# Optimization experiments

Measured on AMD Instinct MI355X. Metric: run time of the kernel, lower is better.

Reference implementation:

```python
import jax, jax.numpy as jnp
import numpy as np

L = 256  # label-space bound (labels 0..L-1, 0 = background)

def setup_inputs() -> dict:
    key = jax.random.key(0)
    k1, k2 = jax.random.split(key)
    H = W = 4096
    pred = jax.random.randint(k1, (H, W), 0, L, dtype=jnp.int32)
    gt = jax.random.randint(k2, (H, W), 0, L, dtype=jnp.int32)
    return {"pred_labels_mask": pred, "gt_labels_mask": gt}

def reference(pred_labels_mask, gt_labels_mask):
    p = pred_labels_mask.reshape(-1).astype(jnp.int32)
    g = gt_labels_mask.reshape(-1).astype(jnp.int32)
    # Label co-occurrence (confusion) matrix via a single scatter-add histogram.
    C = jnp.zeros((L * L,), jnp.int32).at[g * L + p].add(1).reshape(L, L)
    gt_size = C.sum(axis=1)    # full pixel count per gt label
    pred_size = C.sum(axis=0)  # full pixel count per pred label
    gt_present = (gt_size > 0).at[0].set(False)
    pred_present = (pred_size > 0).at[0].set(False)
    num_gt = gt_present.sum()
    num_pred = pred_present.sum()
    # intersections restricted to nonzero gt and nonzero pred labels
    Cnz = C.at[0, :].set(0).at[:, 0].set(0)
    overlap = Cnz > 0
    pairs = overlap.sum()                     # every overlapping (gt,pred) pair is either tp or ns
    ea = (overlap.sum(axis=0) > 1).sum()      # preds overlapping more than one gt
    # match condition: intersection > 0.5*gt_size  <=>  2*inter > gt_size (exact int compare).
    # At most one pred can majority-cover a gt, so argmax identifies it.
    M = (2 * Cnz) > gt_size[:, None]
    best_p = jnp.argmax(M, axis=1)
    has = M.any(axis=1)
    inter = jnp.take_along_axis(Cnz, best_p[:, None], axis=1)[:, 0]
    # Greedy matching in ascending gt-label order (torch.unique order); a pred may match once.
    def step(carry, gl):
        used, tp, seg_sum = carry
        pl = best_p[gl]
        ok = has[gl] & (~used[pl])
        union = gt_size[gl] + pred_size[pl] - inter[gl]
        iou = inter[gl].astype(jnp.float32) / jnp.maximum(union, 1).astype(jnp.float32)
        seg_sum = seg_sum + jnp.where(ok, iou, 0.0)
        used = used.at[pl].set(used[pl] | ok)
        return (used, tp + ok.astype(jnp.int32), seg_sum), None
    init = (jnp.zeros((L,), bool), jnp.int32(0), jnp.float32(0.0))
    (used, tp, seg_sum), _ = jax.lax.scan(step, init, jnp.arange(1, L))
    ng = jnp.maximum(num_gt, 1).astype(jnp.float32)
    seg = seg_sum / ng  # mean over SEG array of length num_gt (zeros for unmatched gts)
    ns = pairs - tp
    fn = num_gt - tp
    fp = num_pred - tp
    det = 1.0 - (fp + fn + ns + ea).astype(jnp.float32) / ng
    both_empty = (num_gt == 0) & (num_pred == 0)
    any_empty = (num_gt == 0) | (num_pred == 0)
    seg = jnp.where(both_empty, 1.0, jnp.where(any_empty, 0.0, seg))
    det = jnp.where(both_empty, 1.0, jnp.where(any_empty, 0.0, det))
    return seg.astype(jnp.float32), det.astype(jnp.float32)
```

## Files before the change

kernel.cpp:

```cpp
#include <hip/hip_runtime.h>

#define LBL 256
#define NBINS (LBL * LBL)
#define NWORDS (NBINS / 2)
#define NQUADS (NWORDS / 4)
#define HIST_BLOCKS 256
#define HIST_THREADS 1024

typedef int vint4 __attribute__((ext_vector_type(4)));

__global__ __launch_bounds__(HIST_THREADS, 4)
void hist_priv_kernel(const int* __restrict__ pred, const int* __restrict__ gt,
                      unsigned int* __restrict__ partial, int n4, int n) {
    __shared__ unsigned int h[NWORDS];
    const int t = threadIdx.x;
    #pragma unroll
    for (int i = t; i < NWORDS; i += HIST_THREADS) h[i] = 0u;
    __syncthreads();

    const vint4* p4 = (const vint4*)pred;
    const vint4* g4 = (const vint4*)gt;
    const int stride = HIST_BLOCKS * HIST_THREADS;
    int i = blockIdx.x * HIST_THREADS + t;
    for (; i + 3 * stride < n4; i += 4 * stride) {
        vint4 pa = __builtin_nontemporal_load(&p4[i]);
        vint4 ga = __builtin_nontemporal_load(&g4[i]);
        vint4 pb = __builtin_nontemporal_load(&p4[i + stride]);
        vint4 gb = __builtin_nontemporal_load(&g4[i + stride]);
        vint4 pc = __builtin_nontemporal_load(&p4[i + 2 * stride]);
        vint4 gc = __builtin_nontemporal_load(&g4[i + 2 * stride]);
        vint4 pd = __builtin_nontemporal_load(&p4[i + 3 * stride]);
        vint4 gd = __builtin_nontemporal_load(&g4[i + 3 * stride]);
        int b;
        b = (ga.x << 8) | pa.x; atomicAdd(&h[b >> 1], 1u << ((b & 1) << 4));
        b = (ga.y << 8) | pa.y; atomicAdd(&h[b >> 1], 1u << ((b & 1) << 4));
        b = (ga.z << 8) | pa.z; atomicAdd(&h[b >> 1], 1u << ((b & 1) << 4));
        b = (ga.w << 8) | pa.w; atomicAdd(&h[b >> 1], 1u << ((b & 1) << 4));
        b = (gb.x << 8) | pb.x; atomicAdd(&h[b >> 1], 1u << ((b & 1) << 4));
        b = (gb.y << 8) | pb.y; atomicAdd(&h[b >> 1], 1u << ((b & 1) << 4));
        b = (gb.z << 8) | pb.z; atomicAdd(&h[b >> 1], 1u << ((b & 1) << 4));
        b = (gb.w << 8) | pb.w; atomicAdd(&h[b >> 1], 1u << ((b & 1) << 4));
        b = (gc.x << 8) | pc.x; atomicAdd(&h[b >> 1], 1u << ((b & 1) << 4));
        b = (gc.y << 8) | pc.y; atomicAdd(&h[b >> 1], 1u << ((b & 1) << 4));
        b = (gc.z << 8) | pc.z; atomicAdd(&h[b >> 1], 1u << ((b & 1) << 4));
        b = (gc.w << 8) | pc.w; atomicAdd(&h[b >> 1], 1u << ((b & 1) << 4));
        b = (gd.x << 8) | pd.x; atomicAdd(&h[b >> 1], 1u << ((b & 1) << 4));
        b = (gd.y << 8) | pd.y; atomicAdd(&h[b >> 1], 1u << ((b & 1) << 4));
        b = (gd.z << 8) | pd.z; atomicAdd(&h[b >> 1], 1u << ((b & 1) << 4));
        b = (gd.w << 8) | pd.w; atomicAdd(&h[b >> 1], 1u << ((b & 1) << 4));
    }
    for (; i < n4; i += stride) {
        vint4 p = p4[i];
        vint4 g = g4[i];
        int b;
        b = (g.x << 8) | p.x; atomicAdd(&h[b >> 1], 1u << ((b & 1) << 4));
        b = (g.y << 8) | p.y; atomicAdd(&h[b >> 1], 1u << ((b & 1) << 4));
        b = (g.z << 8) | p.z; atomicAdd(&h[b >> 1], 1u << ((b & 1) << 4));
        b = (g.w << 8) | p.w; atomicAdd(&h[b >> 1], 1u << ((b & 1) << 4));
    }
    if (blockIdx.x == 0 && t == 0) {
        for (int j = n4 * 4; j < n; ++j) {
            int b = (gt[j] << 8) | pred[j];
            atomicAdd(&h[b >> 1], 1u << ((b & 1) << 4));
        }
    }
    __syncthreads();
    uint4* dst = (uint4*)(partial + (size_t)blockIdx.x * NWORDS);
    const uint4* src = (const uint4*)h;
    #pragma unroll
    for (int j = t; j < NQUADS; j += HIST_THREADS) dst[j] = src[j];
}

__global__ __launch_bounds__(256)
void reduce_kernel(const unsigned int* __restrict__ partial, int* __restrict__ C,
                   int* __restrict__ meta) {
    __shared__ int acc[256];
    __shared__ int red[4], redp[4];
    __shared__ int s_gs, s_rp, s_best, s_inter;
    const int t = threadIdx.x;
    const int r = blockIdx.x;
    acc[t] = 0;
    if (t == 0) { s_best = 0; s_inter = 0; }
    __syncthreads();

    const int qlocal = t & 31;
    const int q = r * 32 + qlocal;
    const int pg = t >> 5;
    const uint4* p4 = (const uint4*)partial;
    int s0 = 0, s1 = 0, s2 = 0, s3 = 0, s4 = 0, s5 = 0, s6 = 0, s7 = 0;
    #pragma unroll 8
    for (int k = 0; k < 32; ++k) {
        uint4 v = p4[(size_t)(pg * 32 + k) * NQUADS + q];
        s0 += (int)(v.x & 0xFFFFu); s1 += (int)(v.x >> 16);
        s2 += (int)(v.y & 0xFFFFu); s3 += (int)(v.y >> 16);
        s4 += (int)(v.z & 0xFFFFu); s5 += (int)(v.z >> 16);
        s6 += (int)(v.w & 0xFFFFu); s7 += (int)(v.w >> 16);
    }
    const int cb = qlocal * 8;
    atomicAdd(&acc[cb + 0], s0); atomicAdd(&acc[cb + 1], s1);
    atomicAdd(&acc[cb + 2], s2); atomicAdd(&acc[cb + 3], s3);
    atomicAdd(&acc[cb + 4], s4); atomicAdd(&acc[cb + 5], s5);
    atomicAdd(&acc[cb + 6], s6); atomicAdd(&acc[cb + 7], s7);
    __syncthreads();

    const int v = acc[t];
    if (t < 64) ((int4*)(C + r * LBL))[t] = ((const int4*)acc)[t];

    int ssum = v;
    int pcnt = (r >= 1 && t >= 1 && v > 0) ? 1 : 0;
    #pragma unroll
    for (int m = 32; m >= 1; m >>= 1) {
        ssum += __shfl_xor(ssum, m);
        pcnt += __shfl_xor(pcnt, m);
    }
    if ((t & 63) == 0) { red[t >> 6] = ssum; redp[t >> 6] = pcnt; }
    __syncthreads();
    if (t == 0) {
        s_gs = red[0] + red[1] + red[2] + red[3];
        s_rp = redp[0] + redp[1] + redp[2] + redp[3];
    }
    __syncthreads();
    const int gs = s_gs;
    if (r >= 1 && t >= 1 && 2 * v > gs) { s_best = t; s_inter = v; }
    __syncthreads();
    if (t == 0) {
        meta[0 * LBL + r] = gs;
        meta[1 * LBL + r] = s_rp;
        meta[2 * LBL + r] = s_best;
        meta[3 * LBL + r] = s_inter;
        meta[4 * LBL + r] = (s_best > 0) ? 1 : 0;
    }
}

__global__ __launch_bounds__(1024)
void finalize_kernel(const int* __restrict__ C, const int* __restrict__ meta,
                     float* __restrict__ out) {
    __shared__ int colsum[1024], colcnt4[1024];
    __shared__ int pred_size[LBL], colcnt[LBL];
    __shared__ unsigned char used_s[LBL];
    __shared__ int s_ngt, s_npred, s_pairs, s_ea;
    const int t = threadIdx.x;
    if (t == 0) { s_ngt = 0; s_npred = 0; s_pairs = 0; s_ea = 0; }
    if (t < LBL) used_s[t] = 0;

    const int c = t & 255, qg = t >> 8;
    int cs = 0, cc = 0;
    #pragma unroll 8
    for (int g0 = 0; g0 < 64; ++g0) {
        int row = qg * 64 + g0;
        int v = C[row * LBL + c];
        cs += v;
        cc += (row >= 1 && c >= 1 && v > 0) ? 1 : 0;
    }
    colsum[t] = cs;
    colcnt4[t] = cc;
    __syncthreads();
    if (t < LBL) {
        pred_size[t] = colsum[t] + colsum[256 + t] + colsum[512 + t] + colsum[768 + t];
        colcnt[t]   = colcnt4[t] + colcnt4[256 + t] + colcnt4[512 + t] + colcnt4[768 + t];
    }
    __syncthreads();
    if (t >= 1 && t < LBL) {
        if (meta[0 * LBL + t] > 0) atomicAdd(&s_ngt, 1);
        if (pred_size[t] > 0) atomicAdd(&s_npred, 1);
        if (colcnt[t] > 1) atomicAdd(&s_ea, 1);
        int rp = meta[1 * LBL + t];
        if (rp) atomicAdd(&s_pairs, rp);
    }
    __syncthreads();

    if (t == 0) {
        const int num_gt = s_ngt, num_pred = s_npred, pairs = s_pairs, ea = s_ea;
        int tp = 0;
        float seg_sum = 0.0f;
        for (int gl = 1; gl < LBL; ++gl) {
            if (meta[4 * LBL + gl]) {
                int pl = meta[2 * LBL + gl];
                if (!used_s[pl]) {
                    int uni = meta[0 * LBL + gl] + pred_size[pl] - meta[3 * LBL + gl];
                    if (uni < 1) uni = 1;
                    seg_sum += (float)meta[3 * LBL + gl] / (float)uni;
                    used_s[pl] = 1;
                    tp++;
                }
            }
        }
        float ng = (float)(num_gt >= 1 ? num_gt : 1);
        float seg = seg_sum / ng;
        int ns = pairs - tp;
        int fn = num_gt - tp;
        int fp_ = num_pred - tp;
        float det = 1.0f - (float)(fp_ + fn + ns + ea) / ng;
        bool both_empty = (num_gt == 0) && (num_pred == 0);
        bool any_empty = (num_gt == 0) || (num_pred == 0);
        if (both_empty) { seg = 1.0f; det = 1.0f; }
        else if (any_empty) { seg = 0.0f; det = 0.0f; }
        out[0] = seg;
        out[1] = det;
    }
}

__global__ void hist_atomic_kernel(const int* __restrict__ pred, const int* __restrict__ gt,
                                   int* __restrict__ C, int n4, int n) {
    int idx = blockIdx.x * blockDim.x + threadIdx.x;
    int stride = gridDim.x * blockDim.x;
    const vint4* p4 = (const vint4*)pred;
    const vint4* g4 = (const vint4*)gt;
    for (int i = idx; i < n4; i += stride) {
        vint4 p = p4[i];
        vint4 g = g4[i];
        atomicAdd(&C[(g.x << 8) + p.x], 1);
        atomicAdd(&C[(g.y << 8) + p.y], 1);
        atomicAdd(&C[(g.z << 8) + p.z], 1);
        atomicAdd(&C[(g.w << 8) + p.w], 1);
    }
    if (idx == 0)
        for (int i = n4 * 4; i < n; ++i) atomicAdd(&C[(gt[i] << 8) + pred[i]], 1);
}

__global__ __launch_bounds__(1024)
void finalize_full_kernel(const int* __restrict__ C, float* __restrict__ out) {
    __shared__ int scratch[1024];
    __shared__ int gt_size[LBL], pred_size[LBL];
    __shared__ int best_p[LBL], inter_s[LBL], colcnt[LBL];
    __shared__ unsigned char has_s[LBL], used_s[LBL];
    __shared__ int s_pairs, s_ngt, s_npred, s_ea;
    const int t = threadIdx.x;
    if (t == 0) { s_pairs = 0; s_ngt = 0; s_npred = 0; s_ea = 0; }
    if (t < LBL) { best_p[t] = 0; inter_s[t] = 0; colcnt[t] = 0; has_s[t] = 0; used_s[t] = 0; }
    const int4* C4 = (const int4*)C;
    const int r = t >> 2, q = t & 3;
    int s = 0;
    #pragma unroll
    for (int j = 0; j < 16; ++j) {
        int4 v = C4[r * 64 + q * 16 + j];
        s += v.x + v.y + v.z + v.w;
    }
    scratch[t] = s;
    __syncthreads();
    if (t < LBL)
        gt_size[t] = scratch[4 * t] + scratch[4 * t + 1] + scratch[4 * t + 2] + scratch[4 * t + 3];
    __syncthreads();
    {
        const int c = t & 255, q2 = t >> 8;
        int cs = 0, cc = 0;
        #pragma unroll 8
        for (int g0 = 0; g0 < 64; ++g0) {
            int row = q2 * 64 + g0;
            int v = C[row * LBL + c];
            cs += v;
            cc += (row >= 1 && c >= 1 && v > 0) ? 1 : 0;
        }
        scratch[t] = cs;
        if (cc) atomicAdd(&colcnt[c], cc);
    }
    if (r >= 1) {
        const int gs = gt_size[r];
        int rp = 0;
        #pragma unroll
        for (int j = 0; j < 16; ++j) {
            int4 v = C4[r * 64 + q * 16 + j];
            int cb = q * 64 + 4 * j;
            if (cb >= 1) {
                if (v.x > 0) rp++;
                if (2 * v.x > gs) { has_s[r] = 1; best_p[r] = cb; inter_s[r] = v.x; }
            }
            if (v.y > 0) rp++;
            if (2 * v.y > gs) { has_s[r] = 1; best_p[r] = cb + 1; inter_s[r] = v.y; }
            if (v.z > 0) rp++;
            if (2 * v.z > gs) { has_s[r] = 1; best_p[r] = cb + 2; inter_s[r] = v.z; }
            if (v.w > 0) rp++;
            if (2 * v.w > gs) { has_s[r] = 1; best_p[r] = cb + 3; inter_s[r] = v.w; }
        }
        if (rp) atomicAdd(&s_pairs, rp);
    }
    __syncthreads();
    if (t < LBL)
        pred_size[t] = scratch[t] + scratch[256 + t] + scratch[512 + t] + scratch[768 + t];
    __syncthreads();
    if (t >= 1 && t < LBL) {
        if (gt_size[t] > 0) atomicAdd(&s_ngt, 1);
        if (pred_size[t] > 0) atomicAdd(&s_npred, 1);
        if (colcnt[t] > 1) atomicAdd(&s_ea, 1);
    }
    __syncthreads();
    if (t == 0) {
        const int num_gt = s_ngt, num_pred = s_npred, pairs = s_pairs, ea = s_ea;
        int tp = 0;
        float seg_sum = 0.0f;
        for (int gl = 1; gl < LBL; ++gl) {
            if (has_s[gl]) {
                int pl = best_p[gl];
                if (!used_s[pl]) {
                    int uni = gt_size[gl] + pred_size[pl] - inter_s[gl];
                    if (uni < 1) uni = 1;
                    seg_sum += (float)inter_s[gl] / (float)uni;
                    used_s[pl] = 1;
                    tp++;
                }
            }
        }
        float ng = (float)(num_gt >= 1 ? num_gt : 1);
        float seg = seg_sum / ng;
        int ns = pairs - tp;
        int fn = num_gt - tp;
        int fp_ = num_pred - tp;
        float det = 1.0f - (float)(fp_ + fn + ns + ea) / ng;
        bool both_empty = (num_gt == 0) && (num_pred == 0);
        bool any_empty = (num_gt == 0) || (num_pred == 0);
        if (both_empty) { seg = 1.0f; det = 1.0f; }
        else if (any_empty) { seg = 0.0f; det = 0.0f; }
        out[0] = seg;
        out[1] = det;
    }
}

extern "C" void kernel_launch(void* const* d_in, const int* in_sizes, int n_in,
                              void* d_out, int out_size, void* d_ws, size_t ws_size,
                              hipStream_t stream) {
    const int* pred = (const int*)d_in[0];
    const int* gt = (const int*)d_in[1];
    float* out = (float*)d_out;
    const int n = in_sizes[0];
    const int n4 = n / 4;

    const size_t part_bytes = (size_t)HIST_BLOCKS * NWORDS * sizeof(unsigned int);
    const size_t c_bytes = (size_t)NBINS * sizeof(int);
    const size_t meta_bytes = 5 * LBL * sizeof(int);
    if (ws_size >= part_bytes + c_bytes + meta_bytes) {
        unsigned int* partial = (unsigned int*)d_ws;
        int* C = (int*)((char*)d_ws + part_bytes);
        int* meta = (int*)((char*)d_ws + part_bytes + c_bytes);
        hist_priv_kernel<<<HIST_BLOCKS, HIST_THREADS, 0, stream>>>(pred, gt, partial, n4, n);
        reduce_kernel<<<LBL, 256, 0, stream>>>(partial, C, meta);
        finalize_kernel<<<1, 1024, 0, stream>>>(C, meta, out);
    } else {
        int* C = (int*)d_ws;
        (void)hipMemsetAsync(C, 0, c_bytes, stream);
        hist_atomic_kernel<<<2048, 256, 0, stream>>>(pred, gt, C, n4, n);
        finalize_full_kernel<<<1, 1024, 0, stream>>>(C, out);
    }
}
```

Before: 169.5 us.

## Fuse finalize into reduce via last-block ticket and widen histogram load batch

Removes the separate single-block finalize kernel and the full confusion-matrix write. Each reduce block atomically adds its column sums and column counts into a small aux buffer, writes its per-row metadata, and takes a ticket. The last block to finish then runs the greedy matching. The histogram loop now batches 8 vector loads per iteration instead of 4 and drops the nontemporal hints. Aux zeroing moves into the histogram kernel. This saves one launch and a 256 KB round trip, at the cost of global atomics, fences and higher register pressure.

```diff
diff --git a/kernel.cpp b/kernel.cpp
--- a/kernel.cpp
+++ b/kernel.cpp
@@ -7,13 +7,25 @@
 #define HIST_BLOCKS 256
 #define HIST_THREADS 1024
 
+#define AUX_COUNTER 0
+#define AUX_COLSUM 64
+#define AUX_COLCNT 320
+#define AUX_GTSIZE 576
+#define AUX_RP 832
+#define AUX_BEST 1088
+#define AUX_INTER 1344
+#define AUX_ZERO_INTS 576
+#define AUX_INTS 1600
+
 typedef int vint4 __attribute__((ext_vector_type(4)));
 
 __global__ __launch_bounds__(HIST_THREADS, 4)
 void hist_priv_kernel(const int* __restrict__ pred, const int* __restrict__ gt,
-                      unsigned int* __restrict__ partial, int n4, int n) {
+                      unsigned int* __restrict__ partial, int* __restrict__ aux,
+                      int n4, int n) {
     __shared__ unsigned int h[NWORDS];
     const int t = threadIdx.x;
+    if (blockIdx.x == 0 && t < AUX_ZERO_INTS) aux[t] = 0;
     #pragma unroll
     for (int i = t; i < NWORDS; i += HIST_THREADS) h[i] = 0u;
     __syncthreads();
@@ -22,32 +34,21 @@
     const vint4* g4 = (const vint4*)gt;
     const int stride = HIST_BLOCKS * HIST_THREADS;
     int i = blockIdx.x * HIST_THREADS + t;
-    for (; i + 3 * stride < n4; i += 4 * stride) {
-        vint4 pa = __builtin_nontemporal_load(&p4[i]);
-        vint4 ga = __builtin_nontemporal_load(&g4[i]);
-        vint4 pb = __builtin_nontemporal_load(&p4[i + stride]);
-        vint4 gb = __builtin_nontemporal_load(&g4[i + stride]);
-        vint4 pc = __builtin_nontemporal_load(&p4[i + 2 * stride]);
-        vint4 gc = __builtin_nontemporal_load(&g4[i + 2 * stride]);
-        vint4 pd = __builtin_nontemporal_load(&p4[i + 3 * stride]);
-        vint4 gd = __builtin_nontemporal_load(&g4[i + 3 * stride]);
-        int b;
-        b = (ga.x << 8) | pa.x; atomicAdd(&h[b >> 1], 1u << ((b & 1) << 4));
-        b = (ga.y << 8) | pa.y; atomicAdd(&h[b >> 1], 1u << ((b & 1) << 4));
-        b = (ga.z << 8) | pa.z; atomicAdd(&h[b >> 1], 1u << ((b & 1) << 4));
-        b = (ga.w << 8) | pa.w; atomicAdd(&h[b >> 1], 1u << ((b & 1) << 4));
-        b = (gb.x << 8) | pb.x; atomicAdd(&h[b >> 1], 1u << ((b & 1) << 4));
-        b = (gb.y << 8) | pb.y; atomicAdd(&h[b >> 1], 1u << ((b & 1) << 4));
-        b = (gb.z << 8) | pb.z; atomicAdd(&h[b >> 1], 1u << ((b & 1) << 4));
-        b = (gb.w << 8) | pb.w; atomicAdd(&h[b >> 1], 1u << ((b & 1) << 4));
-        b = (gc.x << 8) | pc.x; atomicAdd(&h[b >> 1], 1u << ((b & 1) << 4));
-        b = (gc.y << 8) | pc.y; atomicAdd(&h[b >> 1], 1u << ((b & 1) << 4));
-        b = (gc.z << 8) | pc.z; atomicAdd(&h[b >> 1], 1u << ((b & 1) << 4));
-        b = (gc.w << 8) | pc.w; atomicAdd(&h[b >> 1], 1u << ((b & 1) << 4));
-        b = (gd.x << 8) | pd.x; atomicAdd(&h[b >> 1], 1u << ((b & 1) << 4));
-        b = (gd.y << 8) | pd.y; atomicAdd(&h[b >> 1], 1u << ((b & 1) << 4));
-        b = (gd.z << 8) | pd.z; atomicAdd(&h[b >> 1], 1u << ((b & 1) << 4));
-        b = (gd.w << 8) | pd.w; atomicAdd(&h[b >> 1], 1u << ((b & 1) << 4));
+    for (; i + 7 * stride < n4; i += 8 * stride) {
+        vint4 pv[8], gv[8];
+        #pragma unroll
+        for (int u = 0; u < 8; ++u) {
+            pv[u] = p4[i + u * stride];
+            gv[u] = g4[i + u * stride];
+        }
+        #pragma unroll
+        for (int u = 0; u < 8; ++u) {
+            int b;
+            b = (gv[u].x << 8) | pv[u].x; atomicAdd(&h[b >> 1], 1u << ((b & 1) << 4));
+            b = (gv[u].y << 8) | pv[u].y; atomicAdd(&h[b >> 1], 1u << ((b & 1) << 4));
+            b = (gv[u].z << 8) | pv[u].z; atomicAdd(&h[b >> 1], 1u << ((b & 1) << 4));
+            b = (gv[u].w << 8) | pv[u].w; atomicAdd(&h[b >> 1], 1u << ((b & 1) << 4));
+        }
     }
     for (; i < n4; i += stride) {
         vint4 p = p4[i];
@@ -72,11 +73,11 @@
 }
 
 __global__ __launch_bounds__(256)
-void reduce_kernel(const unsigned int* __restrict__ partial, int* __restrict__ C,
-                   int* __restrict__ meta) {
+void reduce_finalize_kernel(const unsigned int* __restrict__ partial,
+                            int* __restrict__ aux, float* __restrict__ out) {
     __shared__ int acc[256];
     __shared__ int red[4], redp[4];
-    __shared__ int s_gs, s_rp, s_best, s_inter;
+    __shared__ int s_gs, s_rp, s_best, s_inter, s_last;
     const int t = threadIdx.x;
     const int r = blockIdx.x;
     acc[t] = 0;
@@ -104,7 +105,8 @@
     __syncthreads();
 
     const int v = acc[t];
-    if (t < 64) ((int4*)(C + r * LBL))[t] = ((const int4*)acc)[t];
+    if (v) atomicAdd(&aux[AUX_COLSUM + t], v);
+    if (r >= 1 && t >= 1 && v > 0) atomicAdd(&aux[AUX_COLCNT + t], 1);
 
     int ssum = v;
     int pcnt = (r >= 1 && t >= 1 && v > 0) ? 1 : 0;
@@ -120,69 +122,53 @@
         s_rp = redp[0] + redp[1] + redp[2] + redp[3];
     }
     __syncthreads();
-    const int gs = s_gs;
-    if (r >= 1 && t >= 1 && 2 * v > gs) { s_best = t; s_inter = v; }
+    if (r >= 1 && t >= 1 && 2 * v > s_gs) { s_best = t; s_inter = v; }
     __syncthreads();
     if (t == 0) {
-        meta[0 * LBL + r] = gs;
-        meta[1 * LBL + r] = s_rp;
-        meta[2 * LBL + r] = s_best;
-        meta[3 * LBL + r] = s_inter;
-        meta[4 * LBL + r] = (s_best > 0) ? 1 : 0;
-    }
-}
-
-__global__ __launch_bounds__(1024)
-void finalize_kernel(const int* __restrict__ C, const int* __restrict__ meta,
-                     float* __restrict__ out) {
-    __shared__ int colsum[1024], colcnt4[1024];
-    __shared__ int pred_size[LBL], colcnt[LBL];
-    __shared__ unsigned char used_s[LBL];
+        aux[AUX_GTSIZE + r] = s_gs;
+        aux[AUX_RP + r] = s_rp;
+        aux[AUX_BEST + r] = s_best;
+        aux[AUX_INTER + r] = s_inter;
+        __threadfence();
+        int ticket = atomicAdd(&aux[AUX_COUNTER], 1);
+        s_last = (ticket == (int)gridDim.x - 1) ? 1 : 0;
+    }
+    __syncthreads();
+    if (!s_last) return;
+    __threadfence();
+
+    __shared__ int gt_size[LBL], pred_size[LBL], best[LBL], inter[LBL];
+    __shared__ int rp_a[LBL], colcnt[LBL];
+    __shared__ unsigned char used[LBL];
     __shared__ int s_ngt, s_npred, s_pairs, s_ea;
-    const int t = threadIdx.x;
     if (t == 0) { s_ngt = 0; s_npred = 0; s_pairs = 0; s_ea = 0; }
-    if (t < LBL) used_s[t] = 0;
-
-    const int c = t & 255, qg = t >> 8;
-    int cs = 0, cc = 0;
-    #pragma unroll 8
-    for (int g0 = 0; g0 < 64; ++g0) {
-        int row = qg * 64 + g0;
-        int v = C[row * LBL + c];
-        cs += v;
-        cc += (row >= 1 && c >= 1 && v > 0) ? 1 : 0;
-    }
-    colsum[t] = cs;
-    colcnt4[t] = cc;
-    __syncthreads();
-    if (t < LBL) {
-        pred_size[t] = colsum[t] + colsum[256 + t] + colsum[512 + t] + colsum[768 + t];
-        colcnt[t]   = colcnt4[t] + colcnt4[256 + t] + colcnt4[512 + t] + colcnt4[768 + t];
-    }
-    __syncthreads();
-    if (t >= 1 && t < LBL) {
-        if (meta[0 * LBL + t] > 0) atomicAdd(&s_ngt, 1);
+    used[t & 255] = 0;
+    gt_size[t]   = __hip_atomic_load(&aux[AUX_GTSIZE + t], __ATOMIC_RELAXED, __HIP_MEMORY_SCOPE_AGENT);
+    rp_a[t]      = __hip_atomic_load(&aux[AUX_RP + t],     __ATOMIC_RELAXED, __HIP_MEMORY_SCOPE_AGENT);
+    best[t]      = __hip_atomic_load(&aux[AUX_BEST + t],   __ATOMIC_RELAXED, __HIP_MEMORY_SCOPE_AGENT);
+    inter[t]     = __hip_atomic_load(&aux[AUX_INTER + t],  __ATOMIC_RELAXED, __HIP_MEMORY_SCOPE_AGENT);
+    pred_size[t] = __hip_atomic_load(&aux[AUX_COLSUM + t], __ATOMIC_RELAXED, __HIP_MEMORY_SCOPE_AGENT);
+    colcnt[t]    = __hip_atomic_load(&aux[AUX_COLCNT + t], __ATOMIC_RELAXED, __HIP_MEMORY_SCOPE_AGENT);
+    __syncthreads();
+    if (t >= 1) {
+        if (gt_size[t] > 0) atomicAdd(&s_ngt, 1);
         if (pred_size[t] > 0) atomicAdd(&s_npred, 1);
         if (colcnt[t] > 1) atomicAdd(&s_ea, 1);
-        int rp = meta[1 * LBL + t];
-        if (rp) atomicAdd(&s_pairs, rp);
-    }
-    __syncthreads();
-
+        if (rp_a[t]) atomicAdd(&s_pairs, rp_a[t]);
+    }
+    __syncthreads();
     if (t == 0) {
         const int num_gt = s_ngt, num_pred = s_npred, pairs = s_pairs, ea = s_ea;
         int tp = 0;
         float seg_sum = 0.0f;
         for (int gl = 1; gl < LBL; ++gl) {
-            if (meta[4 * LBL + gl]) {
-                int pl = meta[2 * LBL + gl];
-                if (!used_s[pl]) {
-                    int uni = meta[0 * LBL + gl] + pred_size[pl] - meta[3 * LBL + gl];
-                    if (uni < 1) uni = 1;
-                    seg_sum += (float)meta[3 * LBL + gl] / (float)uni;
-                    used_s[pl] = 1;
-                    tp++;
-                }
+            int pl = best[gl];
+            if (pl > 0 && !used[pl]) {
+                int uni = gt_size[gl] + pred_size[pl] - inter[gl];
+                if (uni < 1) uni = 1;
+                seg_sum += (float)inter[gl] / (float)uni;
+                used[pl] = 1;
+                tp++;
             }
         }
         float ng = (float)(num_gt >= 1 ? num_gt : 1);
@@ -325,18 +311,15 @@
     const int n4 = n / 4;
 
     const size_t part_bytes = (size_t)HIST_BLOCKS * NWORDS * sizeof(unsigned int);
-    const size_t c_bytes = (size_t)NBINS * sizeof(int);
-    const size_t meta_bytes = 5 * LBL * sizeof(int);
-    if (ws_size >= part_bytes + c_bytes + meta_bytes) {
+    const size_t aux_bytes = AUX_INTS * sizeof(int);
+    if (ws_size >= part_bytes + aux_bytes) {
         unsigned int* partial = (unsigned int*)d_ws;
-        int* C = (int*)((char*)d_ws + part_bytes);
-        int* meta = (int*)((char*)d_ws + part_bytes + c_bytes);
-        hist_priv_kernel<<<HIST_BLOCKS, HIST_THREADS, 0, stream>>>(pred, gt, partial, n4, n);
-        reduce_kernel<<<LBL, 256, 0, stream>>>(partial, C, meta);
-        finalize_kernel<<<1, 1024, 0, stream>>>(C, meta, out);
+        int* aux = (int*)((char*)d_ws + part_bytes);
+        hist_priv_kernel<<<HIST_BLOCKS, HIST_THREADS, 0, stream>>>(pred, gt, partial, aux, n4, n);
+        reduce_finalize_kernel<<<LBL, 256, 0, stream>>>(partial, aux, out);
     } else {
         int* C = (int*)d_ws;
-        (void)hipMemsetAsync(C, 0, c_bytes, stream);
+        (void)hipMemsetAsync(C, 0, (size_t)NBINS * sizeof(int), stream);
         hist_atomic_kernel<<<2048, 256, 0, stream>>>(pred, gt, C, n4, n);
         finalize_full_kernel<<<1, 1024, 0, stream>>>(C, out);
     }
```

New measurement: 185.1 us. 9.2% more time.
